# Performance work log

Hardware: AMD Instinct MI355X
Metric: run time of the kernel (lower is better)

The kernel has to match this reference:

```python
import jax, jax.numpy as jnp
import numpy as np

D_MODEL = 1024
NUM_HEADS = 16
HEAD_DIM = D_MODEL // NUM_HEADS


def setup_inputs() -> dict:
    key = jax.random.key(0)
    ks = jax.random.split(key, 10)
    s = 1.0 / np.sqrt(D_MODEL)
    return {
        "x": jax.random.normal(ks[0], (2, 2048, D_MODEL), dtype=jnp.float32),
        "Wq": jax.random.normal(ks[1], (D_MODEL, D_MODEL), dtype=jnp.float32) * s,
        "bq": jnp.zeros((D_MODEL,), jnp.float32),
        "Wk": jax.random.normal(ks[2], (D_MODEL, D_MODEL), dtype=jnp.float32) * s,
        "bk": jnp.zeros((D_MODEL,), jnp.float32),
        "Wv": jax.random.normal(ks[3], (D_MODEL, D_MODEL), dtype=jnp.float32) * s,
        "bv": jnp.zeros((D_MODEL,), jnp.float32),
        "Wo": jax.random.normal(ks[4], (D_MODEL, D_MODEL), dtype=jnp.float32) * s,
        "bo": jnp.zeros((D_MODEL,), jnp.float32),
        "rotary": jax.random.normal(ks[5], (1, 1, HEAD_DIM), dtype=jnp.float32) * 0.02,
    }


def reference(x, Wq, bq, Wk, bk, Wv, bv, Wo, bo, rotary):
    B, S, _ = x.shape
    H, Dh = NUM_HEADS, HEAD_DIM
    q = (x @ Wq + bq).reshape(B, S, H, Dh)
    k = (x @ Wk + bk).reshape(B, S, H, Dh)
    v = (x @ Wv + bv).reshape(B, S, H, Dh)
    # additive learned bias broadcast over (B, S, H) -> rotary has shape (1,1,Dh)
    q_rot = q + rotary[:, :, None, :]  # (B,S,H,Dh)
    scale = 1.0 / jnp.sqrt(jnp.asarray(Dh, jnp.float32))
    attn = jnp.einsum('bqhd,bkhd->bhqk', q_rot, k) * scale
    attn = jax.nn.softmax(attn, axis=-1)  # dropout is identity in eval / p=0
    out = jnp.einsum('bhqk,bkhd->bqhd', attn, v).reshape(B, S, H * Dh)
    return out @ Wo + bo
```

## Files before the change

kernel.cpp:

```cpp
#include <hip/hip_runtime.h>
#include <hip/hip_bf16.h>
#include <hip/hip_fp16.h>
#include <cstdint>

typedef _Float16 f16;
typedef _Float16 f16x4 __attribute__((ext_vector_type(4)));
typedef _Float16 f16x8 __attribute__((ext_vector_type(8)));
typedef __fp16 h16x2 __attribute__((ext_vector_type(2)));
typedef float f32x4 __attribute__((ext_vector_type(4)));

constexpr int D_MODEL = 1024;
constexpr int NH = 16;
constexpr int DH = 64;
constexpr int BATCH = 2;
constexpr int SEQ = 2048;
constexpr int NTOK = BATCH * SEQ;

static __device__ __forceinline__ void gld_lds16(const void* g, void* l) {
  __builtin_amdgcn_global_load_lds(
      (__attribute__((address_space(1))) void*)(g),
      (__attribute__((address_space(3))) void*)(l), 16, 0, 0);
}

static __device__ __forceinline__ f16x4 pack4(float a, float b, float c, float d) {
  h16x2 lo = __builtin_amdgcn_cvt_pkrtz(a, b);
  h16x2 hi = __builtin_amdgcn_cvt_pkrtz(c, d);
  struct { h16x2 x, y; } pr{lo, hi};
  return __builtin_bit_cast(f16x4, pr);
}


__global__ void cvt_x(const float* __restrict__ x, f16* __restrict__ xh) {
  int i = blockIdx.x * blockDim.x + threadIdx.x;
  const float4* p = reinterpret_cast<const float4*>(x) + (size_t)i * 2;
  float4 a = p[0], b = p[1];
  f16x8 o;
  o[0] = (f16)a.x; o[1] = (f16)a.y; o[2] = (f16)a.z; o[3] = (f16)a.w;
  o[4] = (f16)b.x; o[5] = (f16)b.y; o[6] = (f16)b.z; o[7] = (f16)b.w;
  *reinterpret_cast<f16x8*>(xh + (size_t)i * 8) = o;
}

__global__ void cvt_w(const float* __restrict__ Wq, const float* __restrict__ Wk,
                      const float* __restrict__ Wv, const float* __restrict__ Wo,
                      f16* __restrict__ Wqkvt, f16* __restrict__ Wot) {
  __shared__ float tile[32][33];
  int z = blockIdx.z;
  const float* src = (z == 0) ? Wq : (z == 1) ? Wk : (z == 2) ? Wv : Wo;
  f16* dst = (z < 3) ? (Wqkvt + (size_t)z * D_MODEL * D_MODEL) : Wot;
  int n0 = blockIdx.x * 32, k0 = blockIdx.y * 32;
  int tx = threadIdx.x & 31, ty = threadIdx.x >> 5;
#pragma unroll
  for (int j = 0; j < 32; j += 8)
    tile[ty + j][tx] = src[(size_t)(k0 + ty + j) * D_MODEL + n0 + tx];
  __syncthreads();
#pragma unroll
  for (int j = 0; j < 32; j += 8)
    dst[(size_t)(n0 + ty + j) * D_MODEL + k0 + tx] = (f16)tile[tx][ty + j];
}


template <int MODE, int BM>
__global__ __launch_bounds__(256, 3) void gemm128(
    const f16* __restrict__ A, const f16* __restrict__ Bt,
    const float* __restrict__ b0, const float* __restrict__ b1,
    const float* __restrict__ b2, const float* __restrict__ rot,
    f16* __restrict__ oq, f16* __restrict__ ok, f16* __restrict__ ov,
    float* __restrict__ oOut) {
  constexpr int K = 1024;
  constexpr int BK = 64;
  constexpr int MI = BM / 32;
  constexpr int NBY = 4096 / BM;
  constexpr int CBY = NBY / 8;
  __shared__ __align__(16) f16 As[BM * BK];
  __shared__ __align__(16) f16 Bs[128 * BK];
  const int tid = threadIdx.x;
  const int w = tid >> 6, lane = tid & 63;
  const int flat = blockIdx.x;
  const int xcd = flat & 7, i0 = flat >> 3;
  const int by = xcd * CBY + (i0 % CBY);
  const int bx = i0 / CBY;
  const int m0 = by * BM, n0 = bx * 128;
  const int wr = (w >> 1) * (BM / 2), wc = (w & 1) * 64;
  const int lr = lane & 15, lg = lane >> 4;

  f32x4 acc[MI][4] = {};

  auto stage = [&](int kt) {
#pragma unroll
    for (int i = 0; i < MI; ++i) {
      int seg = (w * MI + i) * 64 + lane;
      int row = seg >> 3, c = seg & 7;
      int col = (c ^ (row & 7)) * 8;
      gld_lds16(A + (size_t)(m0 + row) * K + kt + col, &As[seg * 8]);
    }
#pragma unroll
    for (int i = 0; i < 4; ++i) {
      int seg = (w * 4 + i) * 64 + lane;
      int row = seg >> 3, c = seg & 7;
      int col = (c ^ (row & 7)) * 8;
      gld_lds16(Bt + (size_t)(n0 + row) * K + kt + col, &Bs[seg * 8]);
    }
  };

  stage(0);
#pragma unroll 1
  for (int kt = 0; kt < K; kt += BK) {
    __syncthreads();
#pragma unroll
    for (int kk2 = 0; kk2 < 2; ++kk2) {
      f16x8 af[MI], bf[4];
#pragma unroll
      for (int mi = 0; mi < MI; ++mi)
        af[mi] = *reinterpret_cast<const f16x8*>(
            &As[(wr + mi * 16 + lr) * BK + ((kk2 * 4 + lg) ^ (lr & 7)) * 8]);
#pragma unroll
      for (int ni = 0; ni < 4; ++ni)
        bf[ni] = *reinterpret_cast<const f16x8*>(
            &Bs[(wc + ni * 16 + lr) * BK + ((kk2 * 4 + lg) ^ (lr & 7)) * 8]);
#pragma unroll
      for (int mi = 0; mi < MI; ++mi)
#pragma unroll
        for (int ni = 0; ni < 4; ++ni)
          acc[mi][ni] = __builtin_amdgcn_mfma_f32_16x16x32_f16(af[mi], bf[ni], acc[mi][ni], 0, 0, 0);
    }
    __syncthreads();
    if (kt + BK < K) stage(kt + BK);
  }

#pragma unroll
  for (int mi = 0; mi < MI; ++mi) {
    int rowb = m0 + wr + mi * 16 + lg * 4;
#pragma unroll
    for (int ni = 0; ni < 4; ++ni) {
      int col = n0 + wc + ni * 16 + lr;
#pragma unroll
      for (int r = 0; r < 4; ++r) {
        float val = acc[mi][ni][r];
        int m = rowb + r;
        if (MODE == 0) {
          int which = col >> 10, rest = col & 1023;
          int hh = rest >> 6, d = rest & 63;
          int bb = m >> 11, ss = m & 2047;
          if (which == 0) {
            oq[((size_t)(bb * NH + hh) * SEQ + ss) * DH + d] =
                (f16)((val + b0[rest] + rot[d]) * (0.125f * 1.4426950408889634f));
          } else if (which == 1) {
            ok[((size_t)(bb * NH + hh) * SEQ + ss) * DH + d] = (f16)(val + b1[rest]);
          } else {
            ov[((size_t)(bb * NH + hh) * DH + d) * SEQ + ss] = (f16)(val + b2[rest]);
          }
        } else {
          oOut[(size_t)m * D_MODEL + col] = val + b0[col];
        }
      }
    }
  }
}

__global__ __launch_bounds__(512, 2) void attn(
    const f16* __restrict__ Qg, const f16* __restrict__ Kg,
    const f16* __restrict__ Vtg, f16* __restrict__ Og) {
  __shared__ __align__(16) f16 Ks[2][128 * 64];
  __shared__ __align__(16) f16 Vs[2][64 * 128];
  __shared__ __align__(16) f16 Ps[8][2][16 * 64];
  const int tid = threadIdx.x, w = tid >> 6, lane = tid & 63;
  const int lr = lane & 15, lg = lane >> 4;
  const int b = blockIdx.x;
  const int xcd = b & 7, j = b >> 3;
  const int bh = xcd * 4 + (j & 3);
  const int qb = j >> 2;
  const int q0 = qb * 256 + w * 32;
  const f16* Qb = Qg + (size_t)bh * SEQ * DH;
  const f16* Kb = Kg + (size_t)bh * SEQ * DH;
  const f16* Vtb = Vtg + (size_t)bh * DH * SEQ;

  f16x8 aq[2][2];
#pragma unroll
  for (int qf = 0; qf < 2; ++qf)
#pragma unroll
    for (int ks = 0; ks < 2; ++ks)
      aq[qf][ks] = *reinterpret_cast<const f16x8*>(
          Qb + (size_t)(q0 + qf * 16 + lr) * DH + ks * 32 + lg * 8);

  float li[2] = {0.f, 0.f};
  f32x4 accO[2][4] = {};

  auto stage = [&](int buf, int t) {
#pragma unroll
    for (int i = 0; i < 2; ++i) {
      int seg = (w * 2 + i) * 64 + lane;
      int row = seg >> 3, c = seg & 7;
      gld_lds16(Kb + (size_t)(t + row) * DH + (c ^ (row & 7)) * 8, &Ks[buf][seg * 8]);
    }
#pragma unroll
    for (int i = 0; i < 2; ++i) {
      int seg = (w * 2 + i) * 64 + lane;
      int row = seg >> 4, c = seg & 15;
      gld_lds16(Vtb + (size_t)row * SEQ + t + (c ^ (row & 15)) * 8, &Vs[buf][seg * 8]);
    }
  };

  stage(0, 0);
  int cur = 0;
#pragma unroll 1
  for (int t = 0; t < SEQ; t += 128) {
    __syncthreads();
    if (t + 128 < SEQ) stage(cur ^ 1, t + 128);

    f32x4 sc[2][8];
    __builtin_amdgcn_s_setprio(1);
#pragma unroll
    for (int kt = 0; kt < 8; ++kt) {
      f32x4 z0 = {}, z1 = {};
#pragma unroll
      for (int ks = 0; ks < 2; ++ks) {
        f16x8 kf = *reinterpret_cast<const f16x8*>(
            &Ks[cur][(kt * 16 + lr) * 64 + ((ks * 4 + lg) ^ (lr & 7)) * 8]);
        z0 = __builtin_amdgcn_mfma_f32_16x16x32_f16(kf, aq[0][ks], z0, 0, 0, 0);
        z1 = __builtin_amdgcn_mfma_f32_16x16x32_f16(kf, aq[1][ks], z1, 0, 0, 0);
      }
      sc[0][kt] = z0;
      sc[1][kt] = z1;
    }
    __builtin_amdgcn_s_setprio(0);

#pragma unroll
    for (int qf = 0; qf < 2; ++qf) {
      float rs = 0.f;
#pragma unroll
      for (int kt = 0; kt < 8; ++kt)
#pragma unroll
        for (int r = 0; r < 4; ++r) {
          float p = __builtin_amdgcn_exp2f(sc[qf][kt][r]);
          sc[qf][kt][r] = p;
          rs += p;
        }
      rs += __shfl_xor(rs, 16);
      rs += __shfl_xor(rs, 32);
      li[qf] += rs;
    }

#pragma unroll
    for (int h = 0; h < 2; ++h) {
      f16x8 bv[8];
#pragma unroll
      for (int i = 0; i < 8; ++i) {
        int ct = i >> 1, ks = i & 1;
        int c = h * 8 + ks * 4 + lg;
        bv[i] = *reinterpret_cast<const f16x8*>(
            &Vs[cur][(ct * 16 + lr) * 128 + (c ^ lr) * 8]);
      }
#pragma unroll
      for (int qf = 0; qf < 2; ++qf)
#pragma unroll
        for (int kt2 = 0; kt2 < 4; ++kt2) {
          f32x4 s = sc[qf][h * 4 + kt2];
          f16x4 pk = pack4(s[0], s[1], s[2], s[3]);
          int addr = lr * 64 + (((kt2 * 2 + (lg >> 1)) ^ (lr & 7)) * 8) + (lg & 1) * 4;
          *reinterpret_cast<f16x4*>(&Ps[w][qf][addr]) = pk;
        }
#pragma unroll
      for (int qf = 0; qf < 2; ++qf) {
#pragma unroll
        for (int ks = 0; ks < 2; ++ks) {
          f16x8 ap = *reinterpret_cast<const f16x8*>(
              &Ps[w][qf][lr * 64 + ((ks * 4 + lg) ^ (lr & 7)) * 8]);
          __builtin_amdgcn_s_setprio(1);
#pragma unroll
          for (int ct = 0; ct < 4; ++ct)
            accO[qf][ct] = __builtin_amdgcn_mfma_f32_16x16x32_f16(
                bv[ct * 2 + ks], ap, accO[qf][ct], 0, 0, 0);
          __builtin_amdgcn_s_setprio(0);
        }
      }
    }
    cur ^= 1;
  }

  const int bb = bh >> 4, hh = bh & 15;
#pragma unroll
  for (int qf = 0; qf < 2; ++qf) {
    float inv = 1.f / li[qf];
    f16* dst = Og + (size_t)(bb * SEQ + q0 + qf * 16 + lr) * D_MODEL + hh * DH;
#pragma unroll
    for (int ct = 0; ct < 4; ++ct) {
      f16x4 pk = pack4(accO[qf][ct][0] * inv, accO[qf][ct][1] * inv,
                       accO[qf][ct][2] * inv, accO[qf][ct][3] * inv);
      *reinterpret_cast<f16x4*>(dst + ct * 16 + lg * 4) = pk;
    }
  }
}


extern "C" void kernel_launch(void* const* d_in, const int* in_sizes, int n_in,
                              void* d_out, int out_size, void* d_ws, size_t ws_size,
                              hipStream_t stream) {
  const float* x  = (const float*)d_in[0];
  const float* Wq = (const float*)d_in[1];
  const float* bq = (const float*)d_in[2];
  const float* Wk = (const float*)d_in[3];
  const float* bk = (const float*)d_in[4];
  const float* Wv = (const float*)d_in[5];
  const float* bv = (const float*)d_in[6];
  const float* Wo = (const float*)d_in[7];
  const float* bo = (const float*)d_in[8];
  const float* rot = (const float*)d_in[9];

  char* wsb = (char*)d_ws;
  f16* Xh    = (f16*)(wsb);
  f16* Wqkvt = (f16*)(wsb + ((size_t)8 << 20));
  f16* Wot   = (f16*)(wsb + ((size_t)14 << 20));
  f16* Qa    = (f16*)(wsb + ((size_t)16 << 20));
  f16* Ka    = (f16*)(wsb + ((size_t)24 << 20));
  f16* Oa    = (f16*)(wsb + ((size_t)40 << 20));
  f16* Vta   = (f16*)(wsb + ((size_t)48 << 20));

  cvt_x<<<dim3(NTOK * D_MODEL / (8 * 256)), dim3(256), 0, stream>>>(x, Xh);
  cvt_w<<<dim3(32, 32, 4), dim3(256), 0, stream>>>(Wq, Wk, Wv, Wo, Wqkvt, Wot);

  gemm128<0, 128><<<dim3(768), dim3(256), 0, stream>>>(
      Xh, Wqkvt, bq, bk, bv, rot, Qa, Ka, Vta, nullptr);

  attn<<<dim3((SEQ / 256) * BATCH * NH), dim3(512), 0, stream>>>(Qa, Ka, Vta, Oa);

  gemm128<1, 64><<<dim3(512), dim3(256), 0, stream>>>(
      Oa, Wot, bo, nullptr, nullptr, nullptr, nullptr, nullptr, nullptr,
      (float*)d_out);
}
```

Measured before the change: 198.2 us.

## Switch attention to 32x32x16 MFMA and keep P in registers via permlane32 swap

The attention kernel moves from 16x16x32 MFMA tiles to 32x32x16 tiles, so each wave computes 32 query rows per tile with f32x16 accumulators. The softmax probabilities are packed to fp16 and rearranged between lane halves with v_permlane32_swap, then fed straight into the PV MFMA. This removes the per-wave Ps shared-memory round trip and its LDS writes and reads. Launch bounds change from 2 to 1 block per CU to allow more registers, which may reduce occupancy.

```diff
diff --git a/kernel.cpp b/kernel.cpp
--- a/kernel.cpp
+++ b/kernel.cpp
@@ -8,6 +8,7 @@
 typedef _Float16 f16x8 __attribute__((ext_vector_type(8)));
 typedef __fp16 h16x2 __attribute__((ext_vector_type(2)));
 typedef float f32x4 __attribute__((ext_vector_type(4)));
+typedef float f32x16 __attribute__((ext_vector_type(16)));
 
 constexpr int D_MODEL = 1024;
 constexpr int NH = 16;
@@ -27,6 +28,10 @@
   h16x2 hi = __builtin_amdgcn_cvt_pkrtz(c, d);
   struct { h16x2 x, y; } pr{lo, hi};
   return __builtin_bit_cast(f16x4, pr);
+}
+
+static __device__ __forceinline__ int packi(float a, float b) {
+  return __builtin_bit_cast(int, __builtin_amdgcn_cvt_pkrtz(a, b));
 }
 
 
@@ -157,14 +162,13 @@
   }
 }
 
-__global__ __launch_bounds__(512, 2) void attn(
+__global__ __launch_bounds__(512, 1) void attn(
     const f16* __restrict__ Qg, const f16* __restrict__ Kg,
     const f16* __restrict__ Vtg, f16* __restrict__ Og) {
   __shared__ __align__(16) f16 Ks[2][128 * 64];
   __shared__ __align__(16) f16 Vs[2][64 * 128];
-  __shared__ __align__(16) f16 Ps[8][2][16 * 64];
   const int tid = threadIdx.x, w = tid >> 6, lane = tid & 63;
-  const int lr = lane & 15, lg = lane >> 4;
+  const int m = lane & 31, hi = lane >> 5;
   const int b = blockIdx.x;
   const int xcd = b & 7, j = b >> 3;
   const int bh = xcd * 4 + (j & 3);
@@ -174,16 +178,14 @@
   const f16* Kb = Kg + (size_t)bh * SEQ * DH;
   const f16* Vtb = Vtg + (size_t)bh * DH * SEQ;
 
-  f16x8 aq[2][2];
-#pragma unroll
-  for (int qf = 0; qf < 2; ++qf)
-#pragma unroll
-    for (int ks = 0; ks < 2; ++ks)
-      aq[qf][ks] = *reinterpret_cast<const f16x8*>(
-          Qb + (size_t)(q0 + qf * 16 + lr) * DH + ks * 32 + lg * 8);
-
-  float li[2] = {0.f, 0.f};
-  f32x4 accO[2][4] = {};
+  f16x8 aq[4];
+#pragma unroll
+  for (int ds2 = 0; ds2 < 4; ++ds2)
+    aq[ds2] = *reinterpret_cast<const f16x8*>(
+        Qb + (size_t)(q0 + m) * DH + ds2 * 16 + hi * 8);
+
+  float li = 0.f;
+  f32x16 accO[2] = {};
 
   auto stage = [&](int buf, int t) {
 #pragma unroll
@@ -207,88 +209,75 @@
     __syncthreads();
     if (t + 128 < SEQ) stage(cur ^ 1, t + 128);
 
-    f32x4 sc[2][8];
+    f32x16 sc[4];
     __builtin_amdgcn_s_setprio(1);
 #pragma unroll
-    for (int kt = 0; kt < 8; ++kt) {
-      f32x4 z0 = {}, z1 = {};
-#pragma unroll
-      for (int ks = 0; ks < 2; ++ks) {
+    for (int blk = 0; blk < 4; ++blk) {
+      f32x16 z = {};
+#pragma unroll
+      for (int ds2 = 0; ds2 < 4; ++ds2) {
         f16x8 kf = *reinterpret_cast<const f16x8*>(
-            &Ks[cur][(kt * 16 + lr) * 64 + ((ks * 4 + lg) ^ (lr & 7)) * 8]);
-        z0 = __builtin_amdgcn_mfma_f32_16x16x32_f16(kf, aq[0][ks], z0, 0, 0, 0);
-        z1 = __builtin_amdgcn_mfma_f32_16x16x32_f16(kf, aq[1][ks], z1, 0, 0, 0);
+            &Ks[cur][(blk * 32 + m) * 64 + ((ds2 * 2 + hi) ^ (m & 7)) * 8]);
+        z = __builtin_amdgcn_mfma_f32_32x32x16_f16(kf, aq[ds2], z, 0, 0, 0);
       }
-      sc[0][kt] = z0;
-      sc[1][kt] = z1;
+      sc[blk] = z;
     }
     __builtin_amdgcn_s_setprio(0);
 
-#pragma unroll
-    for (int qf = 0; qf < 2; ++qf) {
+    {
       float rs = 0.f;
 #pragma unroll
-      for (int kt = 0; kt < 8; ++kt)
-#pragma unroll
-        for (int r = 0; r < 4; ++r) {
-          float p = __builtin_amdgcn_exp2f(sc[qf][kt][r]);
-          sc[qf][kt][r] = p;
+      for (int blk = 0; blk < 4; ++blk)
+#pragma unroll
+        for (int r = 0; r < 16; ++r) {
+          float p = __builtin_amdgcn_exp2f(sc[blk][r]);
+          sc[blk][r] = p;
           rs += p;
         }
-      rs += __shfl_xor(rs, 16);
       rs += __shfl_xor(rs, 32);
-      li[qf] += rs;
-    }
-
-#pragma unroll
-    for (int h = 0; h < 2; ++h) {
-      f16x8 bv[8];
-#pragma unroll
-      for (int i = 0; i < 8; ++i) {
-        int ct = i >> 1, ks = i & 1;
-        int c = h * 8 + ks * 4 + lg;
-        bv[i] = *reinterpret_cast<const f16x8*>(
-            &Vs[cur][(ct * 16 + lr) * 128 + (c ^ lr) * 8]);
-      }
-#pragma unroll
-      for (int qf = 0; qf < 2; ++qf)
-#pragma unroll
-        for (int kt2 = 0; kt2 < 4; ++kt2) {
-          f32x4 s = sc[qf][h * 4 + kt2];
-          f16x4 pk = pack4(s[0], s[1], s[2], s[3]);
-          int addr = lr * 64 + (((kt2 * 2 + (lg >> 1)) ^ (lr & 7)) * 8) + (lg & 1) * 4;
-          *reinterpret_cast<f16x4*>(&Ps[w][qf][addr]) = pk;
+      li += rs;
+    }
+
+#pragma unroll
+    for (int blk = 0; blk < 4; ++blk) {
+      int pk[8];
+#pragma unroll
+      for (int g = 0; g < 4; ++g)
+#pragma unroll
+        for (int u = 0; u < 2; ++u)
+          pk[g * 2 + u] = packi(sc[blk][g * 4 + 2 * u], sc[blk][g * 4 + 2 * u + 1]);
+#pragma unroll
+      for (int h = 0; h < 2; ++h) {
+        int x0 = pk[4 * h + 0], x1 = pk[4 * h + 1];
+        int y0 = pk[4 * h + 2], y1 = pk[4 * h + 3];
+        asm volatile("v_permlane32_swap_b32 %0, %1" : "+v"(x0), "+v"(y0));
+        asm volatile("v_permlane32_swap_b32 %0, %1" : "+v"(x1), "+v"(y1));
+        struct { int a, b, c, d; } bi{x0, x1, y0, y1};
+        f16x8 bf = __builtin_bit_cast(f16x8, bi);
+        __builtin_amdgcn_s_setprio(1);
+#pragma unroll
+        for (int dt = 0; dt < 2; ++dt) {
+          f16x8 av = *reinterpret_cast<const f16x8*>(
+              &Vs[cur][(dt * 32 + m) * 128 + ((blk * 4 + h * 2 + hi) ^ (m & 15)) * 8]);
+          accO[dt] = __builtin_amdgcn_mfma_f32_32x32x16_f16(av, bf, accO[dt], 0, 0, 0);
         }
-#pragma unroll
-      for (int qf = 0; qf < 2; ++qf) {
-#pragma unroll
-        for (int ks = 0; ks < 2; ++ks) {
-          f16x8 ap = *reinterpret_cast<const f16x8*>(
-              &Ps[w][qf][lr * 64 + ((ks * 4 + lg) ^ (lr & 7)) * 8]);
-          __builtin_amdgcn_s_setprio(1);
-#pragma unroll
-          for (int ct = 0; ct < 4; ++ct)
-            accO[qf][ct] = __builtin_amdgcn_mfma_f32_16x16x32_f16(
-                bv[ct * 2 + ks], ap, accO[qf][ct], 0, 0, 0);
-          __builtin_amdgcn_s_setprio(0);
-        }
+        __builtin_amdgcn_s_setprio(0);
       }
     }
     cur ^= 1;
   }
 
   const int bb = bh >> 4, hh = bh & 15;
-#pragma unroll
-  for (int qf = 0; qf < 2; ++qf) {
-    float inv = 1.f / li[qf];
-    f16* dst = Og + (size_t)(bb * SEQ + q0 + qf * 16 + lr) * D_MODEL + hh * DH;
-#pragma unroll
-    for (int ct = 0; ct < 4; ++ct) {
-      f16x4 pk = pack4(accO[qf][ct][0] * inv, accO[qf][ct][1] * inv,
-                       accO[qf][ct][2] * inv, accO[qf][ct][3] * inv);
-      *reinterpret_cast<f16x4*>(dst + ct * 16 + lg * 4) = pk;
-    }
-  }
+  float inv = 1.f / li;
+  f16* dst = Og + (size_t)(bb * SEQ + q0 + m) * D_MODEL + hh * DH;
+#pragma unroll
+  for (int dt = 0; dt < 2; ++dt)
+#pragma unroll
+    for (int g = 0; g < 4; ++g) {
+      f16x4 pk4 = pack4(accO[dt][g * 4 + 0] * inv, accO[dt][g * 4 + 1] * inv,
+                        accO[dt][g * 4 + 2] * inv, accO[dt][g * 4 + 3] * inv);
+      *reinterpret_cast<f16x4*>(dst + dt * 32 + g * 8 + hi * 4) = pk4;
+    }
 }
 
 
```

After: 193.6 us. 2.3% less time.
